# Performance work log

Hardware: AMD Instinct MI355X
Metric: run time of the kernel (lower is better)

## Reference

```python
import jax, jax.numpy as jnp
import numpy as np

B, N, I, H, NT = 512, 21, 256, 1024, 5  # batch, nodes, input, hidden, node types
EPS = 1e-12


def setup_inputs() -> dict:
    key = jax.random.key(0)
    ks = jax.random.split(key, 8)
    stdv = 1.0 / np.sqrt(H)
    return {
        "input": jax.random.normal(ks[0], (B, N, I), jnp.float32),
        "hx": 0.1 * jax.random.normal(ks[1], (B, N, H), jnp.float32),
        "cx": 0.1 * jax.random.normal(ks[2], (B, N, H), jnp.float32),
        "G": jnp.eye(N, dtype=jnp.float32) + 0.01 * jax.random.normal(ks[3], (N, N), jnp.float32),
        "weight_ih": jax.random.uniform(ks[4], (NT, 4 * H, I), jnp.float32, -stdv, stdv),
        "weight_hh": jax.random.uniform(ks[5], (NT, 4 * H, H), jnp.float32, -stdv, stdv),
        "bias_hh": jax.random.uniform(ks[6], (NT, 4 * H), jnp.float32, -stdv, stdv),
        "node_types": jax.random.randint(ks[7], (N,), 0, NT),
        "t": 3,
    }


def _l1_normalize_rows(g):
    # torch.nn.functional.normalize(g, p=1, dim=1)
    return g / jnp.maximum(jnp.sum(jnp.abs(g), axis=1, keepdims=True), EPS)


def _clockwork_phase(hidden_size, dtype):
    p = jnp.arange(hidden_size, dtype=dtype)
    p = p / p[-1] * 8.0 + 1.0
    return jnp.floor(p)  # values in {1..9}


def reference(input, hx, cx, G, weight_ih, weight_hh, bias_hh, node_types, t):
    # learn_influence=True -> gx = L1-row-normalized G
    gx = _l1_normalize_rows(G)

    # per-node-type weight gather: [N, 4H, I], [N, 4H, H], [N, 4H]
    w_ih = weight_ih[node_types]
    w_hh = weight_hh[node_types]
    b_hh = bias_hh[node_types]

    # gmm: einsum('ndo,bnd->bno', w.transpose(-2,-1), x) == einsum('noi,bni->bno', w, x)
    gates = (jnp.einsum('noi,bni->bno', w_ih, input)
             + jnp.einsum('noh,bnh->bno', w_hh, hx)
             + b_hh)
    # graph influence: matmul(gx, gates) over node dim -> [B, N, 4H]
    gates = jnp.einsum('mn,bno->bmo', gx, gates)

    ingate, forgetgate, cellgate, outgate = jnp.split(gates, 4, axis=2)
    ingate = jax.nn.sigmoid(ingate)
    forgetgate = jax.nn.sigmoid(forgetgate)
    cellgate = jnp.tanh(cellgate)
    outgate = jax.nn.sigmoid(outgate)

    phase = _clockwork_phase(hx.shape[-1], cx.dtype)
    c_mask = (jnp.remainder(jnp.float32(t) + 1.0, phase) < 0.01).astype(cx.dtype)

    cy = c_mask * (forgetgate * cx + ingate * cellgate) + (1.0 - c_mask) * cx
    hy = outgate * jnp.tanh(cy)

    # gx = gx + G_add (=0), then re-normalized because learn_influence=True
    gx_out = _l1_normalize_rows(gx)
    return hy, cy, gx_out
```

## Files before the change

kernel.cpp:

```cpp
#include <hip/hip_runtime.h>
#include <hip/hip_bf16.h>
#include <stdint.h>


typedef __bf16 bf16_t;
typedef __bf16 bf16x8 __attribute__((ext_vector_type(8)));
typedef float f32x4 __attribute__((ext_vector_type(4)));

#define NB 512
#define NN 21
#define NI 256
#define NH 1024
#define KDIM 1280
#define ODIM 4096
#define BNH (512ull * 21 * 1024)

__device__ inline void gld16(const void* g, const void* l) {
  __builtin_amdgcn_global_load_lds(
      (const __attribute__((address_space(1))) unsigned int*)g,
      (__attribute__((address_space(3))) unsigned int*)l, 16, 0, 0);
}

__device__ inline float sigmoid_fast(float x) {
  return 1.0f / (1.0f + __expf(-x));
}
__device__ inline float tanh_fast(float x) {
  float ax = fabsf(x);
  float e = __expf(2.0f * ax);
  float t = 1.0f - 2.0f / (e + 1.0f);
  return copysignf(t, x);
}

__global__ void gx_kernel(const float* __restrict__ G, float* __restrict__ gxw,
                          float* __restrict__ gxout) {
  int m = threadIdx.x;
  if (m < NN) {
    float s = 0.f;
    for (int j = 0; j < NN; j++) s += fabsf(G[m * NN + j]);
    s = fmaxf(s, 1e-12f);
    float row[NN];
    float s2 = 0.f;
    for (int j = 0; j < NN; j++) {
      row[j] = G[m * NN + j] / s;
      s2 += fabsf(row[j]);
    }
    s2 = fmaxf(s2, 1e-12f);
    for (int j = 0; j < NN; j++) {
      gxw[m * NN + j] = row[j];
      gxout[m * NN + j] = row[j] / s2;
    }
  }
}

__global__ __launch_bounds__(256) void pack_w(const float* __restrict__ wih,
                                              const float* __restrict__ whh,
                                              bf16_t* __restrict__ Wc) {
  int idx = blockIdx.x * 256 + threadIdx.x;
  if (idx >= 5 * ODIM * KDIM) return;
  int k = idx % KDIM;
  int row = idx / KDIM;
  float v = (k < NI) ? wih[(size_t)row * NI + k] : whh[(size_t)row * NH + (k - NI)];
  Wc[idx] = (bf16_t)v;
}

__global__ __launch_bounds__(256) void pack_x(const float* __restrict__ input,
                                              const float* __restrict__ hx,
                                              bf16_t* __restrict__ Xc) {
  int idx = blockIdx.x * 256 + threadIdx.x;
  if (idx >= NN * NB * KDIM) return;
  int k = idx % KDIM;
  int rest = idx / KDIM;
  int n = rest / NB;
  int b = rest % NB;
  float v = (k < NI) ? input[((size_t)b * NN + n) * NI + k]
                     : hx[((size_t)b * NN + n) * NH + (k - NI)];
  Xc[idx] = (bf16_t)v;
}

__global__ __launch_bounds__(256) void gemm_bt(const bf16_t* __restrict__ Xc,
                                               const bf16_t* __restrict__ Wc,
                                               const float* __restrict__ bhh,
                                               const int* __restrict__ node_types,
                                               bf16_t* __restrict__ gates) {
  __shared__ bf16_t As[128 * 32];
  __shared__ bf16_t Bs[128 * 32];

  const int n = blockIdx.z;
  const int tau = node_types[n];
  const bf16_t* A = Xc + (size_t)n * NB * KDIM;
  const bf16_t* B = Wc + (size_t)tau * ODIM * KDIM;

  const int tid = threadIdx.x;
  const int m0 = blockIdx.y * 128;
  const int n0 = blockIdx.x * 128;

  const int lane = tid & 63;
  const int wv = tid >> 6;
  const int wm = (wv >> 1) * 64;
  const int wn = (wv & 1) * 64;
  const int r = lane & 15;
  const int quad = lane >> 4;

  f32x4 acc[4][4];
#pragma unroll
  for (int i = 0; i < 4; i++)
#pragma unroll
    for (int j = 0; j < 4; j++) acc[i][j] = {0.f, 0.f, 0.f, 0.f};

  const int srow = tid >> 2;
  const int schunk = (tid & 3) * 8;

  for (int k0 = 0; k0 < KDIM; k0 += 32) {
    gld16(A + (size_t)(m0 + srow) * KDIM + k0 + schunk, (char*)As + tid * 16);
    gld16(A + (size_t)(m0 + 64 + srow) * KDIM + k0 + schunk, (char*)As + 4096 + tid * 16);
    gld16(B + (size_t)(n0 + srow) * KDIM + k0 + schunk, (char*)Bs + tid * 16);
    gld16(B + (size_t)(n0 + 64 + srow) * KDIM + k0 + schunk, (char*)Bs + 4096 + tid * 16);
    __syncthreads();

    bf16x8 af[4], bfr[4];
#pragma unroll
    for (int i = 0; i < 4; i++)
      af[i] = *(const bf16x8*)&As[(wm + i * 16 + r) * 32 + quad * 8];
#pragma unroll
    for (int j = 0; j < 4; j++)
      bfr[j] = *(const bf16x8*)&Bs[(wn + j * 16 + r) * 32 + quad * 8];
#pragma unroll
    for (int i = 0; i < 4; i++)
#pragma unroll
      for (int j = 0; j < 4; j++)
        acc[i][j] = __builtin_amdgcn_mfma_f32_16x16x32_bf16(af[i], bfr[j], acc[i][j], 0, 0, 0);
    __syncthreads();
  }

  float bv[4];
#pragma unroll
  for (int j = 0; j < 4; j++) bv[j] = bhh[tau * ODIM + n0 + wn + j * 16 + r];
#pragma unroll
  for (int i = 0; i < 4; i++) {
    int brow = m0 + wm + i * 16 + quad * 4;
#pragma unroll
    for (int j = 0; j < 4; j++) {
      int o = n0 + wn + j * 16 + r;
#pragma unroll
      for (int reg = 0; reg < 4; reg++) {
        int b = brow + reg;
        gates[((size_t)b * NN + n) * ODIM + o] = (bf16_t)(acc[i][j][reg] + bv[j]);
      }
    }
  }
}

__global__ __launch_bounds__(256) void mix_kernel(const bf16_t* __restrict__ gates,
                                                  const float* __restrict__ gx,
                                                  const float* __restrict__ cx,
                                                  const int* __restrict__ t_ptr,
                                                  float* __restrict__ out) {
  __shared__ float gxs[NN * NN];
  int tid = threadIdx.x;
  for (int i = tid; i < NN * NN; i += 256) gxs[i] = gx[i];
  __syncthreads();

  int idx = blockIdx.x * 256 + tid;
  int b = idx >> 10;
  int h = idx & 1023;

  float vals[NN * 4];
#pragma unroll
  for (int n = 0; n < NN; n++)
#pragma unroll
    for (int g = 0; g < 4; g++)
      vals[n * 4 + g] = (float)gates[((size_t)b * NN + n) * ODIM + g * NH + h];

  int t = t_ptr[0];
  float phase = floorf(((float)h / 1023.0f) * 8.0f + 1.0f);
  float fm = fmodf((float)(t + 1), phase);
  bool cmask = fm < 0.01f;

  for (int m = 0; m < NN; m++) {
    float s0 = 0.f, s1 = 0.f, s2 = 0.f, s3 = 0.f;
#pragma unroll
    for (int n = 0; n < NN; n++) {
      float w = gxs[m * NN + n];
      s0 += w * vals[n * 4 + 0];
      s1 += w * vals[n * 4 + 1];
      s2 += w * vals[n * 4 + 2];
      s3 += w * vals[n * 4 + 3];
    }
    float ig = sigmoid_fast(s0);
    float fg = sigmoid_fast(s1);
    float cg = tanh_fast(s2);
    float og = sigmoid_fast(s3);
    size_t off = ((size_t)b * NN + m) * NH + h;
    float cxv = cx[off];
    float cy = cmask ? (fg * cxv + ig * cg) : cxv;
    float hy = og * tanh_fast(cy);
    out[off] = hy;
    out[BNH + off] = cy;
  }
}

extern "C" void kernel_launch(void* const* d_in, const int* in_sizes, int n_in,
                              void* d_out, int out_size, void* d_ws, size_t ws_size,
                              hipStream_t stream) {
  const float* input = (const float*)d_in[0];
  const float* hx = (const float*)d_in[1];
  const float* cx = (const float*)d_in[2];
  const float* G = (const float*)d_in[3];
  const float* wih = (const float*)d_in[4];
  const float* whh = (const float*)d_in[5];
  const float* bhh = (const float*)d_in[6];
  const int* node_types = (const int*)d_in[7];
  const int* t = (const int*)d_in[8];
  float* out = (float*)d_out;

  char* ws = (char*)d_ws;
  bf16_t* Wc = (bf16_t*)ws;
  bf16_t* Xc = (bf16_t*)(ws + 52428800);
  bf16_t* gates = (bf16_t*)(ws + 79953920);
  float* gxw = (float*)(ws + 168034304);

  gx_kernel<<<1, 64, 0, stream>>>(G, gxw, out + 2 * BNH);
  pack_w<<<(5 * ODIM * KDIM) / 256, 256, 0, stream>>>(wih, whh, Wc);
  pack_x<<<(NN * NB * KDIM) / 256, 256, 0, stream>>>(input, hx, Xc);
  dim3 gg(ODIM / 128, NB / 128, NN);
  gemm_bt<<<gg, 256, 0, stream>>>(Xc, Wc, bhh, node_types, gates);
  mix_kernel<<<(NB * NH) / 256, 256, 0, stream>>>(gates, gxw, cx, t, out);
}
```

Measured before the change: 465.4 us.

## Vectorize pack kernels and split graph mixing from LSTM pointwise stage

```diff
diff --git a/kernel.cpp b/kernel.cpp
--- a/kernel.cpp
+++ b/kernel.cpp
@@ -55,26 +55,37 @@
 __global__ __launch_bounds__(256) void pack_w(const float* __restrict__ wih,
                                               const float* __restrict__ whh,
                                               bf16_t* __restrict__ Wc) {
-  int idx = blockIdx.x * 256 + threadIdx.x;
-  if (idx >= 5 * ODIM * KDIM) return;
-  int k = idx % KDIM;
-  int row = idx / KDIM;
-  float v = (k < NI) ? wih[(size_t)row * NI + k] : whh[(size_t)row * NH + (k - NI)];
-  Wc[idx] = (bf16_t)v;
+  int c = blockIdx.x * 256 + threadIdx.x;
+  int k8 = c % (KDIM / 8);
+  int row = c / (KDIM / 8);
+  int k = k8 * 8;
+  const float* src = (k < NI) ? (wih + (size_t)row * NI + k)
+                              : (whh + (size_t)row * NH + (k - NI));
+  float4 a = *(const float4*)src;
+  float4 b = *(const float4*)(src + 4);
+  bf16x8 o;
+  o[0] = (bf16_t)a.x; o[1] = (bf16_t)a.y; o[2] = (bf16_t)a.z; o[3] = (bf16_t)a.w;
+  o[4] = (bf16_t)b.x; o[5] = (bf16_t)b.y; o[6] = (bf16_t)b.z; o[7] = (bf16_t)b.w;
+  *(bf16x8*)&Wc[(size_t)c * 8] = o;
 }
 
 __global__ __launch_bounds__(256) void pack_x(const float* __restrict__ input,
                                               const float* __restrict__ hx,
                                               bf16_t* __restrict__ Xc) {
-  int idx = blockIdx.x * 256 + threadIdx.x;
-  if (idx >= NN * NB * KDIM) return;
-  int k = idx % KDIM;
-  int rest = idx / KDIM;
+  int c = blockIdx.x * 256 + threadIdx.x;
+  int k8 = c % (KDIM / 8);
+  int rest = c / (KDIM / 8);
   int n = rest / NB;
   int b = rest % NB;
-  float v = (k < NI) ? input[((size_t)b * NN + n) * NI + k]
-                     : hx[((size_t)b * NN + n) * NH + (k - NI)];
-  Xc[idx] = (bf16_t)v;
+  int k = k8 * 8;
+  const float* src = (k < NI) ? (input + ((size_t)b * NN + n) * NI + k)
+                              : (hx + ((size_t)b * NN + n) * NH + (k - NI));
+  float4 a = *(const float4*)src;
+  float4 d = *(const float4*)(src + 4);
+  bf16x8 o;
+  o[0] = (bf16_t)a.x; o[1] = (bf16_t)a.y; o[2] = (bf16_t)a.z; o[3] = (bf16_t)a.w;
+  o[4] = (bf16_t)d.x; o[5] = (bf16_t)d.y; o[6] = (bf16_t)d.z; o[7] = (bf16_t)d.w;
+  *(bf16x8*)&Xc[(size_t)c * 8] = o;
 }
 
 __global__ __launch_bounds__(256) void gemm_bt(const bf16_t* __restrict__ Xc,
@@ -150,53 +161,76 @@
   }
 }
 
-__global__ __launch_bounds__(256) void mix_kernel(const bf16_t* __restrict__ gates,
-                                                  const float* __restrict__ gx,
-                                                  const float* __restrict__ cx,
-                                                  const int* __restrict__ t_ptr,
-                                                  float* __restrict__ out) {
+__global__ __launch_bounds__(256) void mix_lin(bf16_t* __restrict__ gates,
+                                               const float* __restrict__ gx) {
   __shared__ float gxs[NN * NN];
-  int tid = threadIdx.x;
+  __shared__ bf16_t gs[NN * 512];
+  const int tid = threadIdx.x;
   for (int i = tid; i < NN * NN; i += 256) gxs[i] = gx[i];
+  const int b = blockIdx.y;
+  const int o0 = blockIdx.x * 512;
+  const size_t base = (size_t)b * NN * ODIM + o0;
+
+  for (int i = tid; i < NN * 64; i += 256) {
+    int n = i / 64, c = i % 64;
+    *(bf16x8*)&gs[n * 512 + c * 8] = *(const bf16x8*)&gates[base + (size_t)n * ODIM + c * 8];
+  }
   __syncthreads();
 
-  int idx = blockIdx.x * 256 + tid;
-  int b = idx >> 10;
-  int h = idx & 1023;
-
-  float vals[NN * 4];
-#pragma unroll
-  for (int n = 0; n < NN; n++)
-#pragma unroll
-    for (int g = 0; g < 4; g++)
-      vals[n * 4 + g] = (float)gates[((size_t)b * NN + n) * ODIM + g * NH + h];
-
-  int t = t_ptr[0];
-  float phase = floorf(((float)h / 1023.0f) * 8.0f + 1.0f);
-  float fm = fmodf((float)(t + 1), phase);
-  bool cmask = fm < 0.01f;
-
-  for (int m = 0; m < NN; m++) {
-    float s0 = 0.f, s1 = 0.f, s2 = 0.f, s3 = 0.f;
-#pragma unroll
+  for (int i = tid; i < NN * 64; i += 256) {
+    int m = i / 64, c = i % 64;
+    float acc[8];
+#pragma unroll
+    for (int j = 0; j < 8; j++) acc[j] = 0.f;
     for (int n = 0; n < NN; n++) {
       float w = gxs[m * NN + n];
-      s0 += w * vals[n * 4 + 0];
-      s1 += w * vals[n * 4 + 1];
-      s2 += w * vals[n * 4 + 2];
-      s3 += w * vals[n * 4 + 3];
-    }
-    float ig = sigmoid_fast(s0);
-    float fg = sigmoid_fast(s1);
-    float cg = tanh_fast(s2);
-    float og = sigmoid_fast(s3);
-    size_t off = ((size_t)b * NN + m) * NH + h;
-    float cxv = cx[off];
-    float cy = cmask ? (fg * cxv + ig * cg) : cxv;
-    float hy = og * tanh_fast(cy);
-    out[off] = hy;
-    out[BNH + off] = cy;
-  }
+      bf16x8 v = *(const bf16x8*)&gs[n * 512 + c * 8];
+#pragma unroll
+      for (int j = 0; j < 8; j++) acc[j] += w * (float)v[j];
+    }
+    bf16x8 o;
+#pragma unroll
+    for (int j = 0; j < 8; j++) o[j] = (bf16_t)acc[j];
+    *(bf16x8*)&gates[base + (size_t)m * ODIM + c * 8] = o;
+  }
+}
+
+__global__ __launch_bounds__(256) void lstm_pw(const bf16_t* __restrict__ gates,
+                                               const float* __restrict__ cx,
+                                               const int* __restrict__ t_ptr,
+                                               float* __restrict__ out) {
+  int idx = blockIdx.x * 256 + threadIdx.x;
+  int h8 = idx % 128;
+  int bm = idx / 128;
+  int h = h8 * 8;
+  int t = t_ptr[0];
+  size_t gbase = (size_t)bm * ODIM;
+  bf16x8 vi = *(const bf16x8*)&gates[gbase + 0 * NH + h];
+  bf16x8 vf = *(const bf16x8*)&gates[gbase + 1 * NH + h];
+  bf16x8 vc = *(const bf16x8*)&gates[gbase + 2 * NH + h];
+  bf16x8 vo = *(const bf16x8*)&gates[gbase + 3 * NH + h];
+  size_t off = (size_t)bm * NH + h;
+  float4 c0 = *(const float4*)&cx[off];
+  float4 c1 = *(const float4*)&cx[off + 4];
+  float cxv[8] = {c0.x, c0.y, c0.z, c0.w, c1.x, c1.y, c1.z, c1.w};
+  float hy[8], cy[8];
+  float tf = (float)(t + 1);
+#pragma unroll
+  for (int j = 0; j < 8; j++) {
+    float phase = floorf(((float)(h + j)) / 1023.0f * 8.0f + 1.0f);
+    bool cmask = fmodf(tf, phase) < 0.01f;
+    float ig = sigmoid_fast((float)vi[j]);
+    float fg = sigmoid_fast((float)vf[j]);
+    float cg = tanh_fast((float)vc[j]);
+    float og = sigmoid_fast((float)vo[j]);
+    float c = cmask ? (fg * cxv[j] + ig * cg) : cxv[j];
+    cy[j] = c;
+    hy[j] = og * tanh_fast(c);
+  }
+  *(float4*)&out[off] = make_float4(hy[0], hy[1], hy[2], hy[3]);
+  *(float4*)&out[off + 4] = make_float4(hy[4], hy[5], hy[6], hy[7]);
+  *(float4*)&out[BNH + off] = make_float4(cy[0], cy[1], cy[2], cy[3]);
+  *(float4*)&out[BNH + off + 4] = make_float4(cy[4], cy[5], cy[6], cy[7]);
 }
 
 extern "C" void kernel_launch(void* const* d_in, const int* in_sizes, int n_in,
@@ -220,9 +254,11 @@
   float* gxw = (float*)(ws + 168034304);
 
   gx_kernel<<<1, 64, 0, stream>>>(G, gxw, out + 2 * BNH);
-  pack_w<<<(5 * ODIM * KDIM) / 256, 256, 0, stream>>>(wih, whh, Wc);
-  pack_x<<<(NN * NB * KDIM) / 256, 256, 0, stream>>>(input, hx, Xc);
+  pack_w<<<(5 * ODIM * KDIM / 8) / 256, 256, 0, stream>>>(wih, whh, Wc);
+  pack_x<<<(NN * NB * KDIM / 8) / 256, 256, 0, stream>>>(input, hx, Xc);
   dim3 gg(ODIM / 128, NB / 128, NN);
   gemm_bt<<<gg, 256, 0, stream>>>(Xc, Wc, bhh, node_types, gates);
-  mix_kernel<<<(NB * NH) / 256, 256, 0, stream>>>(gates, gxw, cx, t, out);
-}
+  dim3 gm(ODIM / 512, NB);
+  mix_lin<<<gm, 256, 0, stream>>>(gates, gxw);
+  lstm_pw<<<(NB * NN * (NH / 8)) / 256, 256, 0, stream>>>(gates, cx, t, out);
+}
```

After: 458.8 us. About the same (-1.4%).
